# Kernel tuning notes

Measured on AMD Instinct MI355X. Metric: run time of the kernel, lower is better.

Reference implementation:

```python
import jax, jax.numpy as jnp
import numpy as np

N_NODES = 100000
N_EDGES = 1600000
D = 64
NUM_GROUPS = 2


def setup_inputs() -> dict:
    key = jax.random.key(0)
    k_h, k_ws, k_wg, k_src, k_dst, k_grp = jax.random.split(key, 6)
    h = jax.random.normal(k_h, (N_NODES, D), dtype=jnp.float32)
    # nn.Linear(in, out, bias=False) weights have shape [out, in]
    W_self = jax.random.normal(k_ws, (D, D), dtype=jnp.float32) * (1.0 / np.sqrt(D))
    W_groups = jax.random.normal(k_wg, (NUM_GROUPS, D, D), dtype=jnp.float32) * (1.0 / np.sqrt(D))
    src = jax.random.randint(k_src, (N_EDGES,), 0, N_NODES, dtype=jnp.int32)
    dst = jax.random.randint(k_dst, (N_EDGES,), 0, N_NODES, dtype=jnp.int32)
    group_labels = jax.random.randint(k_grp, (N_NODES,), 0, NUM_GROUPS, dtype=jnp.int32)
    return {"h": h, "W_self": W_self, "W_groups": W_groups,
            "src": src, "dst": dst, "group_labels": group_labels}


def reference(h, W_self, W_groups, src, dst, group_labels):
    # h: [N, d_in]; W_self: [d_out, d_in]; W_groups: [G, d_out, d_in]
    # Edge list (src, dst) replaces the DGL graph; message m_e = h[src_e],
    # transformed by W_groups[group[src_e]], scatter-added into dst_e.
    n_nodes = h.shape[0]
    num_groups = W_groups.shape[0]

    h_self = h @ W_self.T                       # [N, d_out]

    h_src = jnp.take(h, src, axis=0)            # [E, d_in] edge gather
    g_src = jnp.take(group_labels, src, axis=0)  # [E]

    h_agg = jnp.zeros((n_nodes, W_groups.shape[1]), dtype=h.dtype)
    for i in range(num_groups):  # small fixed loop over groups
        masked = jnp.where((g_src == i)[:, None], h_src, 0.0)  # [E, d_in]
        # Linearity lets us aggregate first, then transform (same math as
        # transforming each message then scatter_add, but far less compute).
        seg = jax.ops.segment_sum(masked, dst, num_segments=n_nodes)  # [N, d_in]
        h_agg = h_agg + seg @ W_groups[i].T      # [N, d_out]

    return h_self + h_agg
```

## Files before the change

kernel.cpp:

```cpp
#include <hip/hip_runtime.h>

#define N_NODES 100000
#define N_EDGES 1600000
#define D 64
#define NB 784
#define NR 8
#define CAPB_R 384
#define LCAP 64
#define SRC_MASK 0x1FFFF
#define NBB 782

typedef unsigned int u32;
typedef short bfrag8 __attribute__((ext_vector_type(8)));
typedef float f32x4 __attribute__((ext_vector_type(4)));


__device__ inline u32 pk_bf16(float lo, float hi) {
    u32 a = __float_as_uint(lo);
    a = (a + 0x7fffu + ((a >> 16) & 1u)) >> 16;
    u32 b = __float_as_uint(hi);
    b = (b + 0x7fffu + ((b >> 16) & 1u)) & 0xffff0000u;
    return a | b;
}

__global__ __launch_bounds__(256) void prep(const float* __restrict__ h,
                                            const float* __restrict__ W_self,
                                            const float* __restrict__ W_groups,
                                            const int* __restrict__ src,
                                            const int* __restrict__ dst,
                                            const int* __restrict__ grp,
                                            int* __restrict__ bcnt,
                                            int* __restrict__ buckets,
                                            u32* __restrict__ h_bf,
                                            u32* __restrict__ Wc) {
    __shared__ int hist[NB];
    __shared__ int gbase[NB];
    const int tid = threadIdx.x;
    const int bx = blockIdx.x;

    if (bx < NBB) {
        const int r = bx & (NR - 1);
        for (int b = tid; b < NB; b += 256) hist[b] = 0;
        __syncthreads();

        int ent[8], bkt[8], rnk[8];
        const int e0 = bx * 2048;
#pragma unroll
        for (int i = 0; i < 8; ++i) {
            int e = e0 + tid + i * 256;
            if (e < N_EDGES) {
                int s = src[e], d = dst[e];
                int g = grp[s];
                bkt[i] = d >> 7;
                ent[i] = s | (g << 17) | ((d & 127) << 18);
                rnk[i] = atomicAdd(&hist[bkt[i]], 1);
            } else {
                bkt[i] = -1;
            }
        }
        __syncthreads();
        for (int b = tid; b < NB; b += 256) {
            int hc = hist[b];
            gbase[b] = hc ? atomicAdd(&bcnt[b * NR + r], hc) : 0;
        }
        __syncthreads();
#pragma unroll
        for (int i = 0; i < 8; ++i) {
            if (bkt[i] >= 0) {
                int pos = gbase[bkt[i]] + rnk[i];
                if (pos < CAPB_R)
                    buckets[(bkt[i] * NR + r) * CAPB_R + pos] = ent[i];
            }
        }
    } else if (bx < NBB + 12500) {
        int i = (bx - NBB) * 256 + tid;
        float2 v = reinterpret_cast<const float2*>(h)[i];
        h_bf[i] = pk_bf16(v.x, v.y);
    } else {
        for (int idx = tid; idx < 6144; idx += 256) {
            int j = idx / 96, kk = idx - j * 96;
            int k = kk * 2;
            float lo, hi;
            if (k < 64)       { lo = W_self[j * 64 + k];          hi = W_self[j * 64 + k + 1]; }
            else if (k < 128) { lo = W_groups[j * 64 + k - 64];   hi = W_groups[j * 64 + k - 63]; }
            else              { lo = W_groups[4096 + j * 64 + k - 128];
                                hi = W_groups[4096 + j * 64 + k - 127]; }
            Wc[j * 96 + kk] = pk_bf16(lo, hi);
        }
    }
}

__global__ __launch_bounds__(256) void gather_gemm(const u32* __restrict__ h_bf,
                                                   const int* __restrict__ bcnt,
                                                   const int* __restrict__ buckets,
                                                   const u32* __restrict__ Wc,
                                                   float* __restrict__ out) {
    __shared__ __align__(16) int lcsr[64 * LCAP];
    __shared__ int cnt0[64];
    __shared__ int cnt1[64];

    const int tid = threadIdx.x;
    const int cb = blockIdx.x >> 1;
    const int sub = blockIdx.x & 1;
    const int nbase = cb * 128 + sub * 64;
    if (nbase >= N_NODES) return;

    if (tid < 64) { cnt0[tid] = 0; cnt1[tid] = 0; }
    __syncthreads();

    for (int r = 0; r < NR; ++r) {
        const int cnt = min(bcnt[cb * NR + r], CAPB_R);
        const int* bp = buckets + (cb * NR + r) * CAPB_R;
        for (int i = tid; i < cnt; i += 256) {
            int e = bp[i];
            if (((e >> 24) & 1) == sub) {
                int nl = (e >> 18) & 63;
                int off = (e & SRC_MASK) * 32;
                if ((e >> 17) & 1) {
                    int s1 = atomicAdd(&cnt1[nl], 1);
                    if (s1 < LCAP) lcsr[nl * LCAP + (LCAP - 1 - s1)] = off;
                } else {
                    int s0 = atomicAdd(&cnt0[nl], 1);
                    if (s0 < LCAP) lcsr[nl * LCAP + s0] = off;
                }
            }
        }
    }
    __syncthreads();

    const int wave = tid >> 6;
    const int lane = tid & 63;
    const int half = lane >> 5;
    const int c = lane & 31;

    for (int q = 0; q < 16; ++q) {
        const int nl = wave * 16 + q;
        const int n = nbase + nl;
        if (n >= N_NODES) continue;

        const int c0 = min(cnt0[nl], LCAP);
        const int c1 = min(cnt1[nl], LCAP);
        float a0l = 0.f, a0h = 0.f, a1l = 0.f, a1h = 0.f;

        int i0 = 0, i1 = 0;
        for (; i0 + 8 <= c0 && i1 + 8 <= c1; i0 += 8, i1 += 8) {
            int offA[4], offB[4];
#pragma unroll
            for (int k = 0; k < 4; ++k) {
                offA[k] = lcsr[nl * LCAP + i0 + 2 * k + half];
                offB[k] = lcsr[nl * LCAP + (LCAP - 1 - (i1 + 2 * k + half))];
            }
            u32 vA[4], vB[4];
#pragma unroll
            for (int k = 0; k < 4; ++k) {
                vA[k] = h_bf[(size_t)offA[k] + c];
                vB[k] = h_bf[(size_t)offB[k] + c];
            }
#pragma unroll
            for (int k = 0; k < 4; ++k) {
                a0l += __uint_as_float(vA[k] << 16);
                a0h += __uint_as_float(vA[k] & 0xffff0000u);
                a1l += __uint_as_float(vB[k] << 16);
                a1h += __uint_as_float(vB[k] & 0xffff0000u);
            }
        }
        for (; i0 + 8 <= c0; i0 += 8) {
#pragma unroll
            for (int k = 0; k < 4; ++k) {
                int off = lcsr[nl * LCAP + i0 + 2 * k + half];
                u32 v = h_bf[(size_t)off + c];
                a0l += __uint_as_float(v << 16);
                a0h += __uint_as_float(v & 0xffff0000u);
            }
        }
        for (; i1 + 8 <= c1; i1 += 8) {
#pragma unroll
            for (int k = 0; k < 4; ++k) {
                int off = lcsr[nl * LCAP + (LCAP - 1 - (i1 + 2 * k + half))];
                u32 v = h_bf[(size_t)off + c];
                a1l += __uint_as_float(v << 16);
                a1h += __uint_as_float(v & 0xffff0000u);
            }
        }
        if (i0 < c0) {
#pragma unroll
            for (int k = 0; k < 4; ++k) {
                int t = i0 + 2 * k + half;
                bool ok = t < c0;
                int off = ok ? lcsr[nl * LCAP + t] : 0;
                u32 v = h_bf[(size_t)off + c];
                a0l += ok ? __uint_as_float(v << 16) : 0.f;
                a0h += ok ? __uint_as_float(v & 0xffff0000u) : 0.f;
            }
        }
        if (i1 < c1) {
#pragma unroll
            for (int k = 0; k < 4; ++k) {
                int t = i1 + 2 * k + half;
                bool ok = t < c1;
                int off = ok ? lcsr[nl * LCAP + (LCAP - 1 - t)] : 0;
                u32 v = h_bf[(size_t)off + c];
                a1l += ok ? __uint_as_float(v << 16) : 0.f;
                a1h += ok ? __uint_as_float(v & 0xffff0000u) : 0.f;
            }
        }

        a0l += __shfl_xor(a0l, 32, 64);
        a0h += __shfl_xor(a0h, 32, 64);
        a1l += __shfl_xor(a1l, 32, 64);
        a1h += __shfl_xor(a1h, 32, 64);

        if (half == 0) {
            lcsr[nl * LCAP + c]      = (int)pk_bf16(a0l, a0h);
            lcsr[nl * LCAP + 32 + c] = (int)pk_bf16(a1l, a1h);
        }
    }
    __syncthreads();

    const int m = lane & 15;
    const int quad = lane >> 4;
    const int nl16 = wave * 16 + m;
    const int arow = nbase + nl16;
    const int ar = (arow < N_NODES) ? arow : (N_NODES - 1);

    union Cvt { uint4 u; bfrag8 s; };
    bfrag8 a[6];
    const u32* ap = h_bf + (size_t)ar * 32 + quad * 4;
#pragma unroll
    for (int ks = 0; ks < 2; ++ks) {
        Cvt cv;
        cv.u = *reinterpret_cast<const uint4*>(ap + ks * 16);
        a[ks] = cv.s;
    }
#pragma unroll
    for (int ks = 2; ks < 6; ++ks) {
        Cvt cv;
        cv.u = *reinterpret_cast<const uint4*>(&lcsr[nl16 * LCAP + (ks - 2) * 16 + quad * 4]);
        a[ks] = cv.s;
    }

    f32x4 acc[4];
#pragma unroll
    for (int jt = 0; jt < 4; ++jt) acc[jt] = (f32x4){0.f, 0.f, 0.f, 0.f};

    const u32* wp = Wc + (size_t)m * 96 + quad * 4;
#pragma unroll
    for (int ks = 0; ks < 6; ++ks) {
#pragma unroll
        for (int jt = 0; jt < 4; ++jt) {
            Cvt cw;
            cw.u = *reinterpret_cast<const uint4*>(wp + jt * 1536 + ks * 16);
            acc[jt] = __builtin_amdgcn_mfma_f32_16x16x32_bf16(a[ks], cw.s, acc[jt], 0, 0, 0);
        }
    }

    const int rbase = nbase + wave * 16 + quad * 4;
#pragma unroll
    for (int jt = 0; jt < 4; ++jt) {
#pragma unroll
        for (int r = 0; r < 4; ++r) {
            int n = rbase + r;
            if (n < N_NODES)
                out[(size_t)n * 64 + jt * 16 + m] = acc[jt][r];
        }
    }
}

extern "C" void kernel_launch(void* const* d_in, const int* in_sizes, int n_in,
                              void* d_out, int out_size, void* d_ws, size_t ws_size,
                              hipStream_t stream) {
    const float* h        = (const float*)d_in[0];
    const float* W_self   = (const float*)d_in[1];
    const float* W_groups = (const float*)d_in[2];
    const int*   src      = (const int*)d_in[3];
    const int*   dst      = (const int*)d_in[4];
    const int*   grp      = (const int*)d_in[5];
    float*       out      = (float*)d_out;

    int* bcnt    = (int*)d_ws;
    int* buckets = bcnt + 8192;
    u32* h_bf    = (u32*)(buckets + NB * NR * CAPB_R);
    u32* Wc      = h_bf + (size_t)N_NODES * 32;

    hipMemsetAsync(bcnt, 0, NB * NR * sizeof(int), stream);

    prep<<<NBB + 12500 + 1, 256, 0, stream>>>(h, W_self, W_groups, src, dst, grp,
                                              bcnt, buckets, h_bf, Wc);
    gather_gemm<<<NB * 2, 256, 0, stream>>>(h_bf, bcnt, buckets, Wc, out);
}
```

Baseline: 187.7 us.

## Split gather blocks to 32 nodes, pad LDS rows, use zero row for tails

Each gather_gemm block now handles 32 nodes instead of 64, so four blocks share each bucket group and the grid doubles. LDS rows are padded to a stride of 68 to avoid bank conflicts. The separate tail and unequal-length loops are replaced by one loop that points masked slots at a zero row appended to h_bf. The MFMA stage splits the output columns across waves, and launch_bounds asks for 8 blocks per CU. This is meant to raise occupancy and cut divergent loop overhead. The cost is that each bucket is scanned four times instead of twice, and some loads fetch the zero row needlessly.

Result: faster. 180.8 us (-3.7%).

```diff
diff --git a/kernel.cpp b/kernel.cpp
--- a/kernel.cpp
+++ b/kernel.cpp
@@ -7,8 +7,10 @@
 #define NR 8
 #define CAPB_R 384
 #define LCAP 64
+#define LSTR 68
 #define SRC_MASK 0x1FFFF
 #define NBB 782
+#define ZOFF (N_NODES * 32)
 
 typedef unsigned int u32;
 typedef short bfrag8 __attribute__((ext_vector_type(8)));
@@ -87,41 +89,48 @@
                                 hi = W_groups[4096 + j * 64 + k - 127]; }
             Wc[j * 96 + kk] = pk_bf16(lo, hi);
         }
-    }
-}
-
-__global__ __launch_bounds__(256) void gather_gemm(const u32* __restrict__ h_bf,
-                                                   const int* __restrict__ bcnt,
-                                                   const int* __restrict__ buckets,
-                                                   const u32* __restrict__ Wc,
-                                                   float* __restrict__ out) {
-    __shared__ __align__(16) int lcsr[64 * LCAP];
-    __shared__ int cnt0[64];
-    __shared__ int cnt1[64];
+        if (tid < 32) h_bf[ZOFF + tid] = 0u;
+    }
+}
+
+__global__ __launch_bounds__(256, 8) void gather_gemm(const u32* __restrict__ h_bf,
+                                                      const int* __restrict__ bcnt,
+                                                      const int* __restrict__ buckets,
+                                                      const u32* __restrict__ Wc,
+                                                      float* __restrict__ out) {
+    __shared__ __align__(16) int lcsr[32 * LSTR];
+    __shared__ int cnt0[32];
+    __shared__ int cnt1[32];
 
     const int tid = threadIdx.x;
-    const int cb = blockIdx.x >> 1;
-    const int sub = blockIdx.x & 1;
-    const int nbase = cb * 128 + sub * 64;
+    const int cb = blockIdx.x >> 2;
+    const int sub = blockIdx.x & 3;
+    const int nbase = cb * 128 + sub * 32;
     if (nbase >= N_NODES) return;
 
-    if (tid < 64) { cnt0[tid] = 0; cnt1[tid] = 0; }
+    if (tid < 32) { cnt0[tid] = 0; cnt1[tid] = 0; }
     __syncthreads();
 
-    for (int r = 0; r < NR; ++r) {
-        const int cnt = min(bcnt[cb * NR + r], CAPB_R);
-        const int* bp = buckets + (cb * NR + r) * CAPB_R;
-        for (int i = tid; i < cnt; i += 256) {
-            int e = bp[i];
-            if (((e >> 24) & 1) == sub) {
-                int nl = (e >> 18) & 63;
-                int off = (e & SRC_MASK) * 32;
-                if ((e >> 17) & 1) {
-                    int s1 = atomicAdd(&cnt1[nl], 1);
-                    if (s1 < LCAP) lcsr[nl * LCAP + (LCAP - 1 - s1)] = off;
-                } else {
-                    int s0 = atomicAdd(&cnt0[nl], 1);
-                    if (s0 < LCAP) lcsr[nl * LCAP + s0] = off;
+    {
+        const int4 cA = *reinterpret_cast<const int4*>(bcnt + cb * NR);
+        const int4 cB = *reinterpret_cast<const int4*>(bcnt + cb * NR + 4);
+        int cns[NR] = { cA.x, cA.y, cA.z, cA.w, cB.x, cB.y, cB.z, cB.w };
+#pragma unroll
+        for (int r = 0; r < NR; ++r) {
+            const int cnt = min(cns[r], CAPB_R);
+            const int* bp = buckets + (cb * NR + r) * CAPB_R;
+            for (int i = tid; i < cnt; i += 256) {
+                int e = bp[i];
+                if (((e >> 23) & 3) == sub) {
+                    int nl = (e >> 18) & 31;
+                    int off = (e & SRC_MASK) * 32;
+                    if ((e >> 17) & 1) {
+                        int s1 = atomicAdd(&cnt1[nl], 1);
+                        if (s1 < LCAP) lcsr[nl * LSTR + (LCAP - 1 - s1)] = off;
+                    } else {
+                        int s0 = atomicAdd(&cnt0[nl], 1);
+                        if (s0 < LCAP) lcsr[nl * LSTR + s0] = off;
+                    }
                 }
             }
         }
@@ -133,75 +142,36 @@
     const int half = lane >> 5;
     const int c = lane & 31;
 
-    for (int q = 0; q < 16; ++q) {
-        const int nl = wave * 16 + q;
-        const int n = nbase + nl;
-        if (n >= N_NODES) continue;
-
+    for (int q = 0; q < 8; ++q) {
+        const int nl = wave * 8 + q;
+        const int base = nl * LSTR;
         const int c0 = min(cnt0[nl], LCAP);
         const int c1 = min(cnt1[nl], LCAP);
+        const int imax = max(c0, c1);
         float a0l = 0.f, a0h = 0.f, a1l = 0.f, a1h = 0.f;
 
-        int i0 = 0, i1 = 0;
-        for (; i0 + 8 <= c0 && i1 + 8 <= c1; i0 += 8, i1 += 8) {
+        for (int i = 0; i < imax; i += 8) {
             int offA[4], offB[4];
 #pragma unroll
             for (int k = 0; k < 4; ++k) {
-                offA[k] = lcsr[nl * LCAP + i0 + 2 * k + half];
-                offB[k] = lcsr[nl * LCAP + (LCAP - 1 - (i1 + 2 * k + half))];
-            }
-            u32 vA[4], vB[4];
+                int t = i + 2 * k + half;
+                int vA = lcsr[base + t];
+                int vB = lcsr[base + (LCAP - 1 - t)];
+                offA[k] = (t < c0) ? vA : ZOFF;
+                offB[k] = (t < c1) ? vB : ZOFF;
+            }
+            u32 xA[4], xB[4];
 #pragma unroll
             for (int k = 0; k < 4; ++k) {
-                vA[k] = h_bf[(size_t)offA[k] + c];
-                vB[k] = h_bf[(size_t)offB[k] + c];
+                xA[k] = h_bf[(size_t)(offA[k] + c)];
+                xB[k] = h_bf[(size_t)(offB[k] + c)];
             }
 #pragma unroll
             for (int k = 0; k < 4; ++k) {
-                a0l += __uint_as_float(vA[k] << 16);
-                a0h += __uint_as_float(vA[k] & 0xffff0000u);
-                a1l += __uint_as_float(vB[k] << 16);
-                a1h += __uint_as_float(vB[k] & 0xffff0000u);
-            }
-        }
-        for (; i0 + 8 <= c0; i0 += 8) {
-#pragma unroll
-            for (int k = 0; k < 4; ++k) {
-                int off = lcsr[nl * LCAP + i0 + 2 * k + half];
-                u32 v = h_bf[(size_t)off + c];
-                a0l += __uint_as_float(v << 16);
-                a0h += __uint_as_float(v & 0xffff0000u);
-            }
-        }
-        for (; i1 + 8 <= c1; i1 += 8) {
-#pragma unroll
-            for (int k = 0; k < 4; ++k) {
-                int off = lcsr[nl * LCAP + (LCAP - 1 - (i1 + 2 * k + half))];
-                u32 v = h_bf[(size_t)off + c];
-                a1l += __uint_as_float(v << 16);
-                a1h += __uint_as_float(v & 0xffff0000u);
-            }
-        }
-        if (i0 < c0) {
-#pragma unroll
-            for (int k = 0; k < 4; ++k) {
-                int t = i0 + 2 * k + half;
-                bool ok = t < c0;
-                int off = ok ? lcsr[nl * LCAP + t] : 0;
-                u32 v = h_bf[(size_t)off + c];
-                a0l += ok ? __uint_as_float(v << 16) : 0.f;
-                a0h += ok ? __uint_as_float(v & 0xffff0000u) : 0.f;
-            }
-        }
-        if (i1 < c1) {
-#pragma unroll
-            for (int k = 0; k < 4; ++k) {
-                int t = i1 + 2 * k + half;
-                bool ok = t < c1;
-                int off = ok ? lcsr[nl * LCAP + (LCAP - 1 - t)] : 0;
-                u32 v = h_bf[(size_t)off + c];
-                a1l += ok ? __uint_as_float(v << 16) : 0.f;
-                a1h += ok ? __uint_as_float(v & 0xffff0000u) : 0.f;
+                a0l += __uint_as_float(xA[k] << 16);
+                a0h += __uint_as_float(xA[k] & 0xffff0000u);
+                a1l += __uint_as_float(xB[k] << 16);
+                a1h += __uint_as_float(xB[k] & 0xffff0000u);
             }
         }
 
@@ -211,21 +181,22 @@
         a1h += __shfl_xor(a1h, 32, 64);
 
         if (half == 0) {
-            lcsr[nl * LCAP + c]      = (int)pk_bf16(a0l, a0h);
-            lcsr[nl * LCAP + 32 + c] = (int)pk_bf16(a1l, a1h);
+            lcsr[base + c]      = (int)pk_bf16(a0l, a0h);
+            lcsr[base + 32 + c] = (int)pk_bf16(a1l, a1h);
         }
     }
     __syncthreads();
 
     const int m = lane & 15;
     const int quad = lane >> 4;
-    const int nl16 = wave * 16 + m;
+    const int rowh = wave & 1;
+    const int jth = wave >> 1;
+    const int nl16 = rowh * 16 + m;
     const int arow = nbase + nl16;
-    const int ar = (arow < N_NODES) ? arow : (N_NODES - 1);
 
     union Cvt { uint4 u; bfrag8 s; };
     bfrag8 a[6];
-    const u32* ap = h_bf + (size_t)ar * 32 + quad * 4;
+    const u32* ap = h_bf + (size_t)arow * 32 + quad * 4;
 #pragma unroll
     for (int ks = 0; ks < 2; ++ks) {
         Cvt cv;
@@ -235,33 +206,31 @@
 #pragma unroll
     for (int ks = 2; ks < 6; ++ks) {
         Cvt cv;
-        cv.u = *reinterpret_cast<const uint4*>(&lcsr[nl16 * LCAP + (ks - 2) * 16 + quad * 4]);
+        cv.u = *reinterpret_cast<const uint4*>(&lcsr[nl16 * LSTR + (ks - 2) * 16 + quad * 4]);
         a[ks] = cv.s;
     }
 
-    f32x4 acc[4];
-#pragma unroll
-    for (int jt = 0; jt < 4; ++jt) acc[jt] = (f32x4){0.f, 0.f, 0.f, 0.f};
+    f32x4 acc[2];
+#pragma unroll
+    for (int jj = 0; jj < 2; ++jj) acc[jj] = (f32x4){0.f, 0.f, 0.f, 0.f};
 
     const u32* wp = Wc + (size_t)m * 96 + quad * 4;
 #pragma unroll
     for (int ks = 0; ks < 6; ++ks) {
 #pragma unroll
-        for (int jt = 0; jt < 4; ++jt) {
+        for (int jj = 0; jj < 2; ++jj) {
             Cvt cw;
-            cw.u = *reinterpret_cast<const uint4*>(wp + jt * 1536 + ks * 16);
-            acc[jt] = __builtin_amdgcn_mfma_f32_16x16x32_bf16(a[ks], cw.s, acc[jt], 0, 0, 0);
-        }
-    }
-
-    const int rbase = nbase + wave * 16 + quad * 4;
-#pragma unroll
-    for (int jt = 0; jt < 4; ++jt) {
+            cw.u = *reinterpret_cast<const uint4*>(wp + (jth * 2 + jj) * 1536 + ks * 16);
+            acc[jj] = __builtin_amdgcn_mfma_f32_16x16x32_bf16(a[ks], cw.s, acc[jj], 0, 0, 0);
+        }
+    }
+
+    const int rbase = nbase + rowh * 16 + quad * 4;
+#pragma unroll
+    for (int jj = 0; jj < 2; ++jj) {
 #pragma unroll
         for (int r = 0; r < 4; ++r) {
-            int n = rbase + r;
-            if (n < N_NODES)
-                out[(size_t)n * 64 + jt * 16 + m] = acc[jt][r];
+            out[(size_t)(rbase + r) * 64 + (jth * 2 + jj) * 16 + m] = acc[jj][r];
         }
     }
 }
@@ -280,11 +249,11 @@
     int* bcnt    = (int*)d_ws;
     int* buckets = bcnt + 8192;
     u32* h_bf    = (u32*)(buckets + NB * NR * CAPB_R);
-    u32* Wc      = h_bf + (size_t)N_NODES * 32;
+    u32* Wc      = h_bf + (size_t)N_NODES * 32 + 32;
 
     hipMemsetAsync(bcnt, 0, NB * NR * sizeof(int), stream);
 
     prep<<<NBB + 12500 + 1, 256, 0, stream>>>(h, W_self, W_groups, src, dst, grp,
                                               bcnt, buckets, h_bf, Wc);
-    gather_gemm<<<NB * 2, 256, 0, stream>>>(h_bf, bcnt, buckets, Wc, out);
-}
+    gather_gemm<<<NB * 4, 256, 0, stream>>>(h_bf, bcnt, buckets, Wc, out);
+}
```
